# Kernel optimization log

Hardware: AMD Instinct MI355X
Metric: run time of the kernel (lower is better)

Reference implementation:

```python
import jax, jax.numpy as jnp
import numpy as np

B, T, E, H = 2, 1024, 1024, 16
D = E // H
HEAVY_RATIO = 0.1
RECENT_RATIO = 0.1
QUANT_RATIO = 0.5  # module-level global `quantized_ratio`
NEG = jnp.finfo(jnp.float32).min


def setup_inputs() -> dict:
    key = jax.random.key(0)
    ks = jax.random.split(key, 10)
    s = 0.02
    hidden_states = jax.random.normal(ks[0], (B, T, E), jnp.float32)
    causal = jnp.tril(jnp.ones((T, T), bool))
    attention_mask = jnp.broadcast_to(jnp.where(causal, 0.0, NEG).astype(jnp.float32)[None, None], (B, 1, T, T))
    lin = lambda k: (jax.random.normal(k, (E, E), jnp.float32) * s)
    return {
        'hidden_states': hidden_states,
        'attention_mask': attention_mask,
        'Wq': lin(ks[1]), 'bq': jnp.zeros((E,), jnp.float32),
        'Wk': lin(ks[2]), 'bk': jnp.zeros((E,), jnp.float32),
        'Wv': lin(ks[3]), 'bv': jnp.zeros((E,), jnp.float32),
        'Wo': lin(ks[4]), 'bo': jnp.zeros((E,), jnp.float32),
    }


def _heavy_hitter_mask(aw, hb):
    # aw: [BH, T, T] masked attn logits. Faithful to local_heavy_hitter_mask
    # (use_gumbel=False path, no padding). Returns bool mask_bottom [BH, T, T].
    BH, Tt, _ = aw.shape
    tmp = jax.nn.softmax(aw, axis=-1)               # fp32 softmax
    acc = tmp[:, :hb, :].sum(axis=1)                # [BH, T]
    acc = acc * (jnp.arange(Tt) < hb)               # zero cols >= hb
    col_lt_hb = (jnp.arange(Tt) < hb)
    init_block = jnp.broadcast_to(col_lt_hb[None, None, :], (BH, hb, Tt))
    row_ids = jnp.arange(BH)[:, None]
    cols = jnp.arange(Tt)

    def step(acc, xs):
        row, t = xs                                  # row: [BH, T], t: scalar index
        tmp_i = jax.nn.softmax(row, axis=-1)
        _, idx = jax.lax.top_k(acc, hb - 1)          # heavy-hitter indices [BH, hb-1]
        mb = jnp.zeros((BH, Tt), bool).at[row_ids, idx].set(True)
        mb = mb | (cols == t)[None, :]               # always keep current token
        acc = (acc + tmp_i) * mb                     # accumulate + evict
        return acc, mb

    ts = jnp.arange(hb, Tt)
    rows = jnp.swapaxes(aw[:, hb:, :], 0, 1)         # [T-hb, BH, T]
    _, mbs = jax.lax.scan(step, acc, (rows, ts))
    mask = jnp.concatenate([init_block, jnp.swapaxes(mbs, 0, 1)], axis=1)
    return jnp.tril(mask)


def reference(hidden_states, attention_mask, Wq, bq, Wk, bk, Wv, bv, Wo, bo):
    scaling = D ** -0.5
    shape = lambda x: jnp.transpose(x.reshape(B, T, H, D), (0, 2, 1, 3)).reshape(B * H, T, D)
    q = shape((hidden_states @ Wq + bq) * scaling)
    k = shape(hidden_states @ Wk + bk)
    v = shape(hidden_states @ Wv + bv)

    aw = jnp.einsum('btd,bsd->bts', q, k)                      # [BH, T, T]
    aw = aw.reshape(B, H, T, T) + attention_mask               # additive causal mask
    aw = jnp.maximum(aw, NEG).reshape(B * H, T, T)

    hb = int(HEAVY_RATIO * T)
    qt = int(hb * QUANT_RATIO)
    hb = hb + qt                                               # inflated heavy budget
    recent = int(RECENT_RATIO * T)

    mask_bottom = _heavy_hitter_mask(jax.lax.stop_gradient(aw), hb)
    recent_mask = jnp.triu(jnp.ones((T, T), bool), -recent)    # recent window
    mask = jnp.tril(mask_bottom | recent_mask[None])

    # torch code recomputes the identical masked logits; reuse aw
    aw = jnp.where(mask, aw, jnp.min(attention_mask))
    probs = jax.nn.softmax(aw, axis=-1)
    out = jnp.einsum('bts,bsd->btd', probs, v)                 # [BH, T, D]
    out = jnp.transpose(out.reshape(B, H, T, D), (0, 2, 1, 3)).reshape(B, T, E)
    return out @ Wo + bo
```

## Files before the change

### kernel.cpp

```cpp
#include <hip/hip_runtime.h>
#include <hip/hip_bf16.h>
#include <stdint.h>

#define TT 1024
#define EE 1024
#define HH 16
#define DD 64
#define BHN 32
#define HB 153
#define RECW 102
#define RING 16
#define INFLT 8
#define NEGF (-3.4028234663852886e38f)

typedef unsigned long long ull;
typedef __attribute__((ext_vector_type(8))) short bf16x8;
typedef __attribute__((ext_vector_type(4))) float f32x4;
typedef __attribute__((address_space(3))) float lds_float;

#define OFF_Q  ((size_t)0)
#define OFF_K  (OFF_Q + (size_t)BHN*TT*DD)
#define OFF_V  (OFF_K + (size_t)BHN*TT*DD)
#define OFF_AW (OFF_V + (size_t)BHN*TT*DD)
#define OFF_M  (OFF_AW + (size_t)BHN*TT*TT)
#define OFF_S  (OFF_M + (size_t)BHN*TT)
#define OFF_AO (OFF_S + (size_t)BHN*TT)
#define OFF_END (OFF_AO + (size_t)BHN*TT*DD)

__device__ __forceinline__ ushort f2bf(float x) {
  unsigned u = __float_as_uint(x);
  u = (u + 0x7FFF + ((u >> 16) & 1)) >> 16;
  return (ushort)u;
}
__device__ __forceinline__ float bf2f(ushort h) {
  return __uint_as_float((unsigned)h << 16);
}

__device__ __forceinline__ void gemm_body(const float* __restrict__ X,
    const float* __restrict__ W, const float* __restrict__ bias,
    float* __restrict__ Y, float scale, int mode, int bx, int by) {
  __shared__ ushort Ah[64][72], Al[64][72];
  __shared__ ushort Bh[64][72], Bl[64][72];
  int tid = threadIdx.x, lane = tid & 63, wid = tid >> 6;
  int r = tid >> 2, c0 = (tid & 3) * 16;
  int r0 = by * 64, n0 = bx * 64;

  f32x4 acc[4];
  #pragma unroll
  for (int nc = 0; nc < 4; ++nc) acc[nc] = (f32x4){0.f, 0.f, 0.f, 0.f};

  for (int k0 = 0; k0 < EE; k0 += 64) {
    __syncthreads();
    {
      const float4* xs = (const float4*)(X + (size_t)(r0 + r) * EE + k0 + c0);
      #pragma unroll
      for (int q4 = 0; q4 < 4; ++q4) {
        float4 v = xs[q4];
        float f[4] = {v.x, v.y, v.z, v.w};
        ushort hi[4], lo[4];
        #pragma unroll
        for (int u = 0; u < 4; ++u) {
          hi[u] = f2bf(f[u]);
          lo[u] = f2bf(f[u] - bf2f(hi[u]));
        }
        *(unsigned*)&Ah[r][c0 + q4*4]     = (unsigned)hi[0] | ((unsigned)hi[1] << 16);
        *(unsigned*)&Ah[r][c0 + q4*4 + 2] = (unsigned)hi[2] | ((unsigned)hi[3] << 16);
        *(unsigned*)&Al[r][c0 + q4*4]     = (unsigned)lo[0] | ((unsigned)lo[1] << 16);
        *(unsigned*)&Al[r][c0 + q4*4 + 2] = (unsigned)lo[2] | ((unsigned)lo[3] << 16);
      }
    }
    {
      const float4* wsrc = (const float4*)(W + (size_t)(k0 + r) * EE + n0 + c0);
      #pragma unroll
      for (int q4 = 0; q4 < 4; ++q4) {
        float4 v = wsrc[q4];
        float f[4] = {v.x, v.y, v.z, v.w};
        #pragma unroll
        for (int u = 0; u < 4; ++u) {
          ushort hi = f2bf(f[u]);
          ushort lo = f2bf(f[u] - bf2f(hi));
          int c = c0 + q4*4 + u;
          Bh[c][r] = hi;
          Bl[c][r] = lo;
        }
      }
    }
    __syncthreads();
    #pragma unroll
    for (int kb = 0; kb < 2; ++kb) {
      bf16x8 ah = *(const bf16x8*)&Ah[wid*16 + (lane & 15)][kb*32 + (lane >> 4)*8];
      bf16x8 al = *(const bf16x8*)&Al[wid*16 + (lane & 15)][kb*32 + (lane >> 4)*8];
      #pragma unroll
      for (int nc = 0; nc < 4; ++nc) {
        bf16x8 bh_ = *(const bf16x8*)&Bh[nc*16 + (lane & 15)][kb*32 + (lane >> 4)*8];
        bf16x8 bl_ = *(const bf16x8*)&Bl[nc*16 + (lane & 15)][kb*32 + (lane >> 4)*8];
        acc[nc] = __builtin_amdgcn_mfma_f32_16x16x32_bf16(ah, bh_, acc[nc], 0, 0, 0);
        acc[nc] = __builtin_amdgcn_mfma_f32_16x16x32_bf16(al, bh_, acc[nc], 0, 0, 0);
        acc[nc] = __builtin_amdgcn_mfma_f32_16x16x32_bf16(ah, bl_, acc[nc], 0, 0, 0);
      }
    }
  }

  int rowbase = wid*16 + (lane >> 4)*4;
  #pragma unroll
  for (int nc = 0; nc < 4; ++nc) {
    int c = n0 + nc*16 + (lane & 15);
    float bv = bias[c];
    #pragma unroll
    for (int qq = 0; qq < 4; ++qq) {
      int rr = r0 + rowbase + qq;
      float val = (acc[nc][qq] + bv) * scale;
      int b_ = rr >> 10, t_ = rr & 1023, h_ = c >> 6, d_ = c & 63;
      if (mode == 1) {
        Y[(((size_t)(b_*HH + h_) * TT) + t_) * DD + d_] = val;
      } else if (mode == 2) {
        ((ushort*)Y)[(((size_t)(b_*HH + h_) * TT) + t_) * DD + d_] = f2bf(val);
      } else {
        Y[(size_t)rr * EE + c] = val;
      }
    }
  }
}

__global__ __launch_bounds__(256) void k_qkv(const float* __restrict__ X,
    const float* __restrict__ Wq, const float* __restrict__ bq,
    const float* __restrict__ Wk, const float* __restrict__ bk,
    const float* __restrict__ Wv, const float* __restrict__ bv,
    float* __restrict__ q, float* __restrict__ k, float* __restrict__ v) {
  int z = blockIdx.z;
  if (z == 0)      gemm_body(X, Wq, bq, q, 0.125f, 1, blockIdx.x, blockIdx.y);
  else if (z == 1) gemm_body(X, Wk, bk, k, 1.0f,   1, blockIdx.x, blockIdx.y);
  else             gemm_body(X, Wv, bv, v, 1.0f,   2, blockIdx.x, blockIdx.y);
}

__global__ __launch_bounds__(256) void k_out(const float* __restrict__ X,
    const float* __restrict__ W, const float* __restrict__ bias,
    float* __restrict__ Y) {
  gemm_body(X, W, bias, Y, 1.0f, 0, blockIdx.x, blockIdx.y);
}

__global__ __launch_bounds__(256) void k_qk_mfma(const float* __restrict__ q,
    const float* __restrict__ k, float* __restrict__ aw) {
  int bh = blockIdx.y, tt = blockIdx.x;
  int t0 = tt * 64;
  int tid = threadIdx.x, lane = tid & 63, wid = tid >> 6;
  int r = tid >> 2, c0 = (tid & 3) * 16;
  __shared__ ushort Qh[64][72], Ql[64][72];
  __shared__ ushort Kh[64][72], Kl[64][72];
  const float* qb = q + (size_t)bh * TT * DD;
  const float* kb = k + (size_t)bh * TT * DD;
  float* awb = aw + (size_t)bh * TT * TT;

  {
    const float4* xs = (const float4*)(qb + (size_t)(t0 + r) * DD + c0);
    #pragma unroll
    for (int q4 = 0; q4 < 4; ++q4) {
      float4 v = xs[q4];
      float f[4] = {v.x, v.y, v.z, v.w};
      ushort hi[4], lo[4];
      #pragma unroll
      for (int u = 0; u < 4; ++u) {
        hi[u] = f2bf(f[u]);
        lo[u] = f2bf(f[u] - bf2f(hi[u]));
      }
      *(unsigned*)&Qh[r][c0 + q4*4]     = (unsigned)hi[0] | ((unsigned)hi[1] << 16);
      *(unsigned*)&Qh[r][c0 + q4*4 + 2] = (unsigned)hi[2] | ((unsigned)hi[3] << 16);
      *(unsigned*)&Ql[r][c0 + q4*4]     = (unsigned)lo[0] | ((unsigned)lo[1] << 16);
      *(unsigned*)&Ql[r][c0 + q4*4 + 2] = (unsigned)lo[2] | ((unsigned)lo[3] << 16);
    }
  }

  for (int st = 0; st <= tt; ++st) {
    __syncthreads();
    {
      const float4* xs = (const float4*)(kb + (size_t)(st * 64 + r) * DD + c0);
      #pragma unroll
      for (int q4 = 0; q4 < 4; ++q4) {
        float4 v = xs[q4];
        float f[4] = {v.x, v.y, v.z, v.w};
        ushort hi[4], lo[4];
        #pragma unroll
        for (int u = 0; u < 4; ++u) {
          hi[u] = f2bf(f[u]);
          lo[u] = f2bf(f[u] - bf2f(hi[u]));
        }
        *(unsigned*)&Kh[r][c0 + q4*4]     = (unsigned)hi[0] | ((unsigned)hi[1] << 16);
        *(unsigned*)&Kh[r][c0 + q4*4 + 2] = (unsigned)hi[2] | ((unsigned)hi[3] << 16);
        *(unsigned*)&Kl[r][c0 + q4*4]     = (unsigned)lo[0] | ((unsigned)lo[1] << 16);
        *(unsigned*)&Kl[r][c0 + q4*4 + 2] = (unsigned)lo[2] | ((unsigned)lo[3] << 16);
      }
    }
    __syncthreads();
    f32x4 acc[4];
    #pragma unroll
    for (int nc = 0; nc < 4; ++nc) acc[nc] = (f32x4){0.f, 0.f, 0.f, 0.f};
    #pragma unroll
    for (int kb2 = 0; kb2 < 2; ++kb2) {
      bf16x8 ah = *(const bf16x8*)&Qh[wid*16 + (lane & 15)][kb2*32 + (lane >> 4)*8];
      bf16x8 al = *(const bf16x8*)&Ql[wid*16 + (lane & 15)][kb2*32 + (lane >> 4)*8];
      #pragma unroll
      for (int nc = 0; nc < 4; ++nc) {
        bf16x8 bh_ = *(const bf16x8*)&Kh[nc*16 + (lane & 15)][kb2*32 + (lane >> 4)*8];
        bf16x8 bl_ = *(const bf16x8*)&Kl[nc*16 + (lane & 15)][kb2*32 + (lane >> 4)*8];
        acc[nc] = __builtin_amdgcn_mfma_f32_16x16x32_bf16(ah, bh_, acc[nc], 0, 0, 0);
        acc[nc] = __builtin_amdgcn_mfma_f32_16x16x32_bf16(al, bh_, acc[nc], 0, 0, 0);
        acc[nc] = __builtin_amdgcn_mfma_f32_16x16x32_bf16(ah, bl_, acc[nc], 0, 0, 0);
      }
    }
    int rowbase = wid*16 + (lane >> 4)*4;
    #pragma unroll
    for (int nc = 0; nc < 4; ++nc) {
      int s = st * 64 + nc*16 + (lane & 15);
      #pragma unroll
      for (int qq = 0; qq < 4; ++qq) {
        int t_ = t0 + rowbase + qq;
        awb[(size_t)t_ * TT + s] = acc[nc][qq];
      }
    }
  }
}

__global__ __launch_bounds__(256) void k_softmax(float* __restrict__ aw) {
  int bh = blockIdx.y;
  int wid = threadIdx.x >> 6, lane = threadIdx.x & 63;
  int t = blockIdx.x * 4 + wid;
  float* row = aw + ((size_t)bh * TT + t) * TT;
  float vals[16];
  float m = NEGF;
  #pragma unroll
  for (int i = 0; i < 16; ++i) {
    int j = lane + 64*i;
    vals[i] = (j <= t) ? row[j] : NEGF;
    m = fmaxf(m, vals[i]);
  }
  for (int o = 32; o; o >>= 1) m = fmaxf(m, __shfl_xor(m, o));
  float s = 0.f;
  #pragma unroll
  for (int i = 0; i < 16; ++i) {
    int j = lane + 64*i;
    if (j <= t) { vals[i] = expf(vals[i] - m); s += vals[i]; }
  }
  for (int o = 32; o; o >>= 1) s += __shfl_xor(s, o);
  float inv = 1.0f / s;
  #pragma unroll
  for (int i = 0; i < 16; ++i) {
    int j = lane + 64*i;
    if (j <= t) row[j] = vals[i] * inv;
  }
}

__global__ __launch_bounds__(256) void k_init_acc(const float* __restrict__ p,
    float* __restrict__ initacc) {
  int bh = blockIdx.x;
  int c = threadIdx.x;
  float val = 0.f;
  if (c < HB) {
    const float* pb = p + (size_t)bh * TT * TT;
    for (int i = c; i < HB; ++i)
      val += pb[(size_t)i * TT + c];
  }
  initacc[(size_t)bh * 256 + c] = val;
}

#define DPP_HOP(ctrl)                                                        \
  {                                                                          \
    unsigned tt = (unsigned)__builtin_amdgcn_update_dpp(                     \
        (int)0xFFFFFFFFu, (int)x, (ctrl), 0xF, 0xF, false);                  \
    x = x < tt ? x : tt;                                                     \
  }
__device__ __forceinline__ unsigned wave_min_u32(unsigned x) {
  DPP_HOP(0x111)
  DPP_HOP(0x112)
  DPP_HOP(0x114)
  DPP_HOP(0x118)
  DPP_HOP(0x142)
  DPP_HOP(0x143)
  return (unsigned)__builtin_amdgcn_readlane((int)x, 63);
}

__device__ __forceinline__ void gload_lds16(const float* gsrc, float* ldst) {
  __builtin_amdgcn_global_load_lds(
      (const __attribute__((address_space(1))) unsigned int*)gsrc,
      (__attribute__((address_space(3))) unsigned int*)ldst,
      16, 0, 0);
}

__global__ __launch_bounds__(64) void k_scan(const float* __restrict__ p,
    const float* __restrict__ initacc, int* __restrict__ evict_g) {
  int bh = blockIdx.x;
  int lane = threadIdx.x;
  const float* pb = p + (size_t)bh * TT * TT;
  __shared__ float ring[RING][TT];
  __shared__ int ev[TT];
  for (int i = lane; i < TT; i += 64) ev[i] = 0x7fffffff;

  bool act2 = lane < (HB - 128);
  int col0 = lane, col1 = 64 + lane, col2 = act2 ? (128 + lane) : 0;
  float sc0 = initacc[(size_t)bh * 256 + lane];
  float sc1 = initacc[(size_t)bh * 256 + 64 + lane];
  float sc2 = act2 ? initacc[(size_t)bh * 256 + 128 + lane] : 0.f;

  unsigned ring_base = (unsigned)(size_t)(lds_float*)&ring[0][0];

  #pragma unroll
  for (int r = 0; r < INFLT; ++r) {
    const float* srcrow = pb + (size_t)(HB + r) * TT;
    float* slotbase = ring[(HB + r) & (RING - 1)];
    #pragma unroll
    for (int j = 0; j < 4; ++j)
      gload_lds16(srcrow + j * 256 + lane * 4, slotbase + j * 256);
  }
  float r0, r1, r2, rd, re;
  {
    unsigned sbase = ring_base + (unsigned)((HB & (RING - 1)) * (TT * 4));
    unsigned a0 = sbase + (unsigned)col0 * 4;
    unsigned a1 = sbase + (unsigned)col1 * 4;
    unsigned a2 = sbase + (unsigned)col2 * 4;
    unsigned ad = sbase + (unsigned)HB * 4;
    unsigned ae = sbase + (unsigned)(HB - 1) * 4;
    asm volatile("s_waitcnt vmcnt(28)");
    asm volatile(
      "ds_read_b32 %0, %5\n\t"
      "ds_read_b32 %1, %6\n\t"
      "ds_read_b32 %2, %7\n\t"
      "ds_read_b32 %3, %8\n\t"
      "ds_read_b32 %4, %9"
      : "=&v"(r0), "=&v"(r1), "=&v"(r2), "=&v"(rd), "=&v"(re)
      : "v"(a0), "v"(a1), "v"(a2), "v"(ad), "v"(ae));
  }
  bool e0p = false, e1p = false, e2p = false;

  for (int t = HB; t < TT; ++t) {
    int tn = (t + 1 < TT) ? (t + 1) : (TT - 1);
    asm volatile("s_waitcnt vmcnt(24)");
    float n0, n1, n2, nd, ne;
    {
      unsigned sbase = ring_base + (unsigned)((tn & (RING - 1)) * (TT * 4));
      unsigned a0 = sbase + (unsigned)col0 * 4;
      unsigned a1 = sbase + (unsigned)col1 * 4;
      unsigned a2 = sbase + (unsigned)col2 * 4;
      unsigned ad = sbase + (unsigned)tn * 4;
      unsigned ae = sbase + (unsigned)t * 4;
      asm volatile(
        "ds_read_b32 %0, %5\n\t"
        "ds_read_b32 %1, %6\n\t"
        "ds_read_b32 %2, %7\n\t"
        "ds_read_b32 %3, %8\n\t"
        "ds_read_b32 %4, %9"
        : "=&v"(n0), "=&v"(n1), "=&v"(n2), "=&v"(nd), "=&v"(ne)
        : "v"(a0), "v"(a1), "v"(a2), "v"(ad), "v"(ae));
    }
    {
      int rn = t + INFLT;
      int rsrc = rn < TT ? rn : TT - 1;
      const float* srcrow = pb + (size_t)rsrc * TT;
      float* slotbase = ring[rn & (RING - 1)];
      #pragma unroll
      for (int j = 0; j < 4; ++j)
        gload_lds16(srcrow + j * 256 + lane * 4, slotbase + j * 256);
    }
    unsigned b0 = __float_as_uint(sc0);
    unsigned b1 = __float_as_uint(sc1);
    unsigned b2 = act2 ? __float_as_uint(sc2) : 0xFFFFFFFFu;
    unsigned mn = b0 < b1 ? b0 : b1; mn = mn < b2 ? mn : b2;
    unsigned mstar = wave_min_u32(mn);
    bool m0 = (b0 == mstar), m1 = (b1 == mstar), m2 = act2 && (b2 == mstar);
    int lcl = (int)m0 + (int)m1 + (int)m2;
    ull bal1 = __ballot(lcl >= 1);
    ull bal2 = __ballot(lcl >= 2);
    bool e0, e1, e2;
    if (bal2 == 0 && __popcll(bal1) == 1) {
      e0 = m0; e1 = m1; e2 = m2;
    } else {
      unsigned c0k = m0 ? (unsigned)(1023 - col0) : 0xFFFFFFFFu;
      unsigned c1k = m1 ? (unsigned)(1023 - col1) : 0xFFFFFFFFu;
      unsigned c2k = m2 ? (unsigned)(1023 - col2) : 0xFFFFFFFFu;
      unsigned cm = c0k < c1k ? c0k : c1k; cm = cm < c2k ? cm : c2k;
      int cstar = 1023 - (int)wave_min_u32(cm);
      e0 = m0 && (col0 == cstar);
      e1 = m1 && (col1 == cstar);
      e2 = m2 && (col2 == cstar);
    }
    asm volatile("s_waitcnt lgkmcnt(5)");
    __builtin_amdgcn_sched_barrier(0);
    float rr0 = e0p ? re : r0;
    float rr1 = e1p ? re : r1;
    float rr2 = e2p ? re : r2;
    if (e0) { ev[col0] = t; col0 = t; sc0 = rd; } else sc0 += rr0;
    if (e1) { ev[col1] = t; col1 = t; sc1 = rd; } else sc1 += rr1;
    if (act2) {
      if (e2) { ev[col2] = t; col2 = t; sc2 = rd; } else sc2 += rr2;
    }
    __builtin_amdgcn_sched_barrier(0);
    e0p = e0; e1p = e1; e2p = e2;
    r0 = n0; r1 = n1; r2 = n2; rd = nd; re = ne;
  }

  asm volatile("s_waitcnt lgkmcnt(0)");
  int4* dst4 = (int4*)(evict_g + (size_t)bh * TT);
  const int4* src4 = (const int4*)ev;
  #pragma unroll
  for (int i = 0; i < 4; ++i) dst4[lane + 64 * i] = src4[lane + 64 * i];
}

__global__ __launch_bounds__(256) void k_pv(const float* __restrict__ p,
    const int* __restrict__ evict_g, const ushort* __restrict__ vbf,
    float* __restrict__ ao) {
  int bh = blockIdx.y, tt = blockIdx.x;
  int tid = threadIdx.x, lane = tid & 63, wid = tid >> 6;
  int t0 = tt * 64;
  __shared__ ushort PA[64][72];
  __shared__ ushort VT[64][72];
  __shared__ float rowsum[64];
  __shared__ int et[TT];
  ((int4*)et)[tid] = ((const int4*)(evict_g + (size_t)bh * TT))[tid];
  if (tid < 64) rowsum[tid] = 0.f;
  const float* pb = p + ((size_t)bh * TT + t0) * TT;
  const ushort* vb = vbf + (size_t)bh * TT * DD;

  f32x4 acc[4];
  #pragma unroll
  for (int nc = 0; nc < 4; ++nc) acc[nc] = (f32x4){0.f, 0.f, 0.f, 0.f};

  int r = tid >> 2;
  int c0 = (tid & 3) * 16;
  int tg = t0 + r;
  __syncthreads();

  for (int st = 0; st <= tt; ++st) {
    const float* prow = pb + (size_t)r * TT + st * 64 + c0;
    float part = 0.f;
    ushort tmp16[16];
    #pragma unroll
    for (int q4 = 0; q4 < 4; ++q4) {
      float4 pv4 = *(const float4*)(prow + q4 * 4);
      float vals[4] = {pv4.x, pv4.y, pv4.z, pv4.w};
      #pragma unroll
      for (int u = 0; u < 4; ++u) {
        int j = st * 64 + c0 + q4 * 4 + u;
        bool allow = (j <= tg) && ((et[j] > tg) || (j + RECW >= tg));
        float mv = allow ? vals[u] : 0.f;
        part += mv;
        tmp16[q4 * 4 + u] = f2bf(mv);
      }
    }
    #pragma unroll
    for (int w2 = 0; w2 < 8; ++w2) {
      unsigned pk = (unsigned)tmp16[w2 * 2] | ((unsigned)tmp16[w2 * 2 + 1] << 16);
      *(unsigned*)&PA[r][c0 + w2 * 2] = pk;
    }
    part += __shfl_xor(part, 1);
    part += __shfl_xor(part, 2);
    if ((tid & 3) == 0) rowsum[r] += part;
    {
      const unsigned* vrow32 = (const unsigned*)(vb + (size_t)(st * 64 + r) * DD + c0);
      #pragma unroll
      for (int u = 0; u < 8; ++u) {
        unsigned vv = vrow32[u];
        VT[c0 + u * 2][r] = (ushort)(vv & 0xFFFF);
        VT[c0 + u * 2 + 1][r] = (ushort)(vv >> 16);
      }
    }
    __syncthreads();
    #pragma unroll
    for (int kb = 0; kb < 2; ++kb) {
      bf16x8 af = *(const bf16x8*)&PA[wid * 16 + (lane & 15)][kb * 32 + (lane >> 4) * 8];
      #pragma unroll
      for (int nc = 0; nc < 4; ++nc) {
        bf16x8 bfr = *(const bf16x8*)&VT[nc * 16 + (lane & 15)][kb * 32 + (lane >> 4) * 8];
        acc[nc] = __builtin_amdgcn_mfma_f32_16x16x32_bf16(af, bfr, acc[nc], 0, 0, 0);
      }
    }
    __syncthreads();
  }

  int b_ = bh >> 4, h_ = bh & 15;
  int rl = wid * 16 + (lane >> 4) * 4;
  #pragma unroll
  for (int nc = 0; nc < 4; ++nc) {
    int d = nc * 16 + (lane & 15);
    #pragma unroll
    for (int qq = 0; qq < 4; ++qq) {
      int rr = rl + qq;
      float outv = acc[nc][qq] / rowsum[rr];
      ao[((size_t)b_ * TT + (t0 + rr)) * EE + h_ * DD + d] = outv;
    }
  }
}

extern "C" void kernel_launch(void* const* d_in, const int* in_sizes, int n_in,
                              void* d_out, int out_size, void* d_ws, size_t ws_size,
                              hipStream_t stream) {
  const float* hs = (const float*)d_in[0];
  const float* Wq = (const float*)d_in[2];
  const float* bq = (const float*)d_in[3];
  const float* Wk = (const float*)d_in[4];
  const float* bk = (const float*)d_in[5];
  const float* Wv = (const float*)d_in[6];
  const float* bv = (const float*)d_in[7];
  const float* Wo = (const float*)d_in[8];
  const float* bo = (const float*)d_in[9];
  float* out = (float*)d_out;

  float* ws = (float*)d_ws;
  float* q  = ws + OFF_Q;
  float* k  = ws + OFF_K;
  float* v  = ws + OFF_V;
  float* aw = ws + OFF_AW;
  float* ao = ws + OFF_AO;
  float* initacc = ws + OFF_END;
  int* evict = (int*)(ws + OFF_END + (size_t)BHN * 256);

  dim3 gqkv(16, 32, 3);
  k_qkv<<<gqkv, 256, 0, stream>>>(hs, Wq, bq, Wk, bk, Wv, bv, q, k, v);

  dim3 gqk(16, BHN);
  k_qk_mfma<<<gqk, 256, 0, stream>>>(q, k, aw);

  dim3 grs(TT/4, BHN);
  k_softmax<<<grs, 256, 0, stream>>>(aw);

  k_init_acc<<<BHN, 256, 0, stream>>>(aw, initacc);

  k_scan<<<BHN, 64, 0, stream>>>(aw, initacc, evict);

  dim3 gpv(16, BHN);
  k_pv<<<gpv, 256, 0, stream>>>(aw, evict, (const ushort*)v, ao);

  dim3 gout(16, 32);
  k_out<<<gout, 256, 0, stream>>>(ao, Wo, bo, out);
}
```

Before: 543.1 us.

## Fuse row softmax into QK^T kernel using online max/sum statistics

The QK^T MFMA kernel now keeps a running max and sum-of-exponentials per row while it produces logit tiles. After the tile loop, each block makes a second pass over its own rows in global memory, turning the stored logits into normalized probabilities. This removes the separate softmax kernel launch and its extra read pass over the logits. In exchange, the QK kernel does extra shuffle reductions, and the normalization pass rereads data the block just wrote. Load across blocks also stays uneven, because blocks near the diagonal end handle more tiles.

```diff
diff --git a/kernel.cpp b/kernel.cpp
--- a/kernel.cpp
+++ b/kernel.cpp
@@ -139,7 +139,7 @@
   gemm_body(X, W, bias, Y, 1.0f, 0, blockIdx.x, blockIdx.y);
 }
 
-__global__ __launch_bounds__(256) void k_qk_mfma(const float* __restrict__ q,
+__global__ __launch_bounds__(256) void k_qk_sm(const float* __restrict__ q,
     const float* __restrict__ k, float* __restrict__ aw) {
   int bh = blockIdx.y, tt = blockIdx.x;
   int t0 = tt * 64;
@@ -147,6 +147,8 @@
   int r = tid >> 2, c0 = (tid & 3) * 16;
   __shared__ ushort Qh[64][72], Ql[64][72];
   __shared__ ushort Kh[64][72], Kl[64][72];
+  __shared__ float rowM[64];
+  __shared__ float rowInv[64];
   const float* qb = q + (size_t)bh * TT * DD;
   const float* kb = k + (size_t)bh * TT * DD;
   float* awb = aw + (size_t)bh * TT * TT;
@@ -169,6 +171,11 @@
       *(unsigned*)&Ql[r][c0 + q4*4 + 2] = (unsigned)lo[2] | ((unsigned)lo[3] << 16);
     }
   }
+
+  int rowbase = wid*16 + (lane >> 4)*4;
+  float mrun[4], srun[4];
+  #pragma unroll
+  for (int qq = 0; qq < 4; ++qq) { mrun[qq] = NEGF; srun[qq] = 0.f; }
 
   for (int st = 0; st <= tt; ++st) {
     __syncthreads();
@@ -207,7 +214,31 @@
         acc[nc] = __builtin_amdgcn_mfma_f32_16x16x32_bf16(ah, bl_, acc[nc], 0, 0, 0);
       }
     }
-    int rowbase = wid*16 + (lane >> 4)*4;
+    bool diag = (st == tt);
+    #pragma unroll
+    for (int qq = 0; qq < 4; ++qq) {
+      int t_ = t0 + rowbase + qq;
+      float tm = NEGF;
+      float mv[4];
+      #pragma unroll
+      for (int nc = 0; nc < 4; ++nc) {
+        int s = st * 64 + nc*16 + (lane & 15);
+        bool ok = !diag || (s <= t_);
+        mv[nc] = ok ? acc[nc][qq] : NEGF;
+        tm = fmaxf(tm, mv[nc]);
+      }
+      #pragma unroll
+      for (int o = 1; o < 16; o <<= 1) tm = fmaxf(tm, __shfl_xor(tm, o));
+      float mnew = fmaxf(mrun[qq], tm);
+      float se = 0.f;
+      #pragma unroll
+      for (int nc = 0; nc < 4; ++nc)
+        se += (mv[nc] > NEGF) ? expf(mv[nc] - mnew) : 0.f;
+      #pragma unroll
+      for (int o = 1; o < 16; o <<= 1) se += __shfl_xor(se, o);
+      srun[qq] = srun[qq] * expf(mrun[qq] - mnew) + se;
+      mrun[qq] = mnew;
+    }
     #pragma unroll
     for (int nc = 0; nc < 4; ++nc) {
       int s = st * 64 + nc*16 + (lane & 15);
@@ -218,34 +249,43 @@
       }
     }
   }
-}
-
-__global__ __launch_bounds__(256) void k_softmax(float* __restrict__ aw) {
-  int bh = blockIdx.y;
-  int wid = threadIdx.x >> 6, lane = threadIdx.x & 63;
-  int t = blockIdx.x * 4 + wid;
-  float* row = aw + ((size_t)bh * TT + t) * TT;
-  float vals[16];
-  float m = NEGF;
-  #pragma unroll
-  for (int i = 0; i < 16; ++i) {
-    int j = lane + 64*i;
-    vals[i] = (j <= t) ? row[j] : NEGF;
-    m = fmaxf(m, vals[i]);
-  }
-  for (int o = 32; o; o >>= 1) m = fmaxf(m, __shfl_xor(m, o));
-  float s = 0.f;
-  #pragma unroll
-  for (int i = 0; i < 16; ++i) {
-    int j = lane + 64*i;
-    if (j <= t) { vals[i] = expf(vals[i] - m); s += vals[i]; }
-  }
-  for (int o = 32; o; o >>= 1) s += __shfl_xor(s, o);
-  float inv = 1.0f / s;
-  #pragma unroll
-  for (int i = 0; i < 16; ++i) {
-    int j = lane + 64*i;
-    if (j <= t) row[j] = vals[i] * inv;
+
+  if ((lane & 15) == 0) {
+    #pragma unroll
+    for (int qq = 0; qq < 4; ++qq) {
+      rowM[rowbase + qq] = mrun[qq];
+      rowInv[rowbase + qq] = 1.0f / srun[qq];
+    }
+  }
+  __syncthreads();
+
+  {
+    int t_ = t0 + r;
+    float m = rowM[r];
+    float inv = rowInv[r];
+    float* rowp = awb + (size_t)t_ * TT;
+    for (int st = 0; st < tt; ++st) {
+      float4* p4 = (float4*)(rowp + st * 64 + c0);
+      #pragma unroll
+      for (int q4 = 0; q4 < 4; ++q4) {
+        float4 v = p4[q4];
+        v.x = expf(v.x - m) * inv;
+        v.y = expf(v.y - m) * inv;
+        v.z = expf(v.z - m) * inv;
+        v.w = expf(v.w - m) * inv;
+        p4[q4] = v;
+      }
+    }
+    {
+      #pragma unroll
+      for (int q4 = 0; q4 < 4; ++q4) {
+        #pragma unroll
+        for (int u = 0; u < 4; ++u) {
+          int j = tt * 64 + c0 + q4 * 4 + u;
+          if (j <= t_) rowp[j] = expf(rowp[j] - m) * inv;
+        }
+      }
+    }
   }
 }
 
@@ -515,10 +555,7 @@
   k_qkv<<<gqkv, 256, 0, stream>>>(hs, Wq, bq, Wk, bk, Wv, bv, q, k, v);
 
   dim3 gqk(16, BHN);
-  k_qk_mfma<<<gqk, 256, 0, stream>>>(q, k, aw);
-
-  dim3 grs(TT/4, BHN);
-  k_softmax<<<grs, 256, 0, stream>>>(aw);
+  k_qk_sm<<<gqk, 256, 0, stream>>>(q, k, aw);
 
   k_init_acc<<<BHN, 256, 0, stream>>>(aw, initacc);
 
```

New measurement: 648.2 us. 1.19x slower.
